# Kernel tuning notes

Hardware: AMD Instinct MI355X
Metric: run time of the kernel (lower is better)

The kernel has to match this reference:

```python
import jax, jax.numpy as jnp
import numpy as np

B, H, W, C = 32, 224, 224, 3
HID = 64


def setup_inputs() -> dict:
    key = jax.random.key(0)
    k0, k1, k2 = jax.random.split(key, 3)
    inputs = jax.random.normal(k0, (B, H, W, C), dtype=jnp.float32)
    # Localization-net dense params. Original uses zeros init (identity transform);
    # we use small random weights plus the identity affine bias so the sampling
    # grid is a nontrivial perturbation of identity.
    w1 = jax.random.normal(k1, (H * W * C, HID), dtype=jnp.float32) * 1e-3
    b1 = jnp.zeros((HID,), dtype=jnp.float32)
    w2 = jax.random.normal(k2, (HID, 6), dtype=jnp.float32) * 1e-2
    b2 = jnp.array([1.0, 0.0, 0.0, 0.0, 1.0, 0.0], dtype=jnp.float32)
    return {"inputs": inputs, "w1": w1, "b1": b1, "w2": w2, "b2": b2}


def _bilinear_sampler(img, x_s, y_s):
    # img: [B,H,W,C]; x_s, y_s: [B,H,W] normalized coords in [-1,1]
    Bn, Hn, Wn, Cn = img.shape
    x = 0.5 * (x_s + 1.0) * (Wn - 1)
    y = 0.5 * (y_s + 1.0) * (Hn - 1)
    x0 = jnp.floor(x).astype(jnp.int32)
    x1 = x0 + 1
    y0 = jnp.floor(y).astype(jnp.int32)
    y1 = y0 + 1
    x0c = jnp.clip(x0, 0, Wn - 1)
    x1c = jnp.clip(x1, 0, Wn - 1)
    y0c = jnp.clip(y0, 0, Hn - 1)
    y1c = jnp.clip(y1, 0, Hn - 1)
    b_idx = jnp.arange(Bn, dtype=jnp.int32)[:, None, None]
    Ia = img[b_idx, y0c, x0c]  # [B,H,W,C]
    Ib = img[b_idx, y1c, x0c]
    Ic = img[b_idx, y0c, x1c]
    Id = img[b_idx, y1c, x1c]
    x0f = x0c.astype(x.dtype)
    x1f = x1c.astype(x.dtype)
    y0f = y0c.astype(y.dtype)
    y1f = y1c.astype(y.dtype)
    wa = ((x1f - x) * (y1f - y))[..., None]
    wb = ((x1f - x) * (y - y0f))[..., None]
    wc = ((x - x0f) * (y1f - y))[..., None]
    wd = ((x - x0f) * (y - y0f))[..., None]
    return wa * Ia + wb * Ib + wc * Ic + wd * Id


def reference(inputs, w1, b1, w2, b2):
    Bn, Hn, Wn, Cn = inputs.shape
    # NOTE: original keras code overwrites the conv branch with flatten(inputs),
    # so the conv/maxpool layers are dead code and omitted. Dropout is identity
    # at inference (training=False).
    flat = inputs.reshape(Bn, -1)
    h = jnp.tanh(flat @ w1 + b1)
    theta = jnp.tanh(h @ w2 + b2).reshape(Bn, 2, 3)
    # affine sampling grid over normalized target coords
    xt, yt = jnp.meshgrid(
        jnp.linspace(-1.0, 1.0, Wn, dtype=inputs.dtype),
        jnp.linspace(-1.0, 1.0, Hn, dtype=inputs.dtype),
    )  # each [H,W]
    grid = jnp.stack([xt.ravel(), yt.ravel(), jnp.ones_like(xt).ravel()])  # [3,H*W]
    batch_grid = jnp.einsum("bij,jk->bik", theta, grid).reshape(Bn, 2, Hn, Wn)
    x_s = batch_grid[:, 0]
    y_s = batch_grid[:, 1]
    return _bilinear_sampler(inputs, x_s, y_s)
```

## Files before the change

### kernel.cpp

```cpp
#include <hip/hip_runtime.h>

#define BATCH 32
#define HDIM 224
#define WDIM 224
#define CDIM 3
#define KTOT (HDIM * WDIM * CDIM)
#define HID 64
#define KCHUNK 384
#define NBLK1 (KTOT / KCHUNK)
#define PIX (HDIM * WDIM)
#define BLK3 (PIX / 256)

__global__ __launch_bounds__(256) void k1_gemm(const float* __restrict__ flat,
                                               const float* __restrict__ w1,
                                               float* __restrict__ hacc) {
    const int tid  = threadIdx.x;
    const int hid  = tid & 63;
    const int bg   = tid >> 6;
    const int bbase = bg * 8;

    float acc[8];
#pragma unroll
    for (int j = 0; j < 8; ++j) acc[j] = 0.0f;

    const int k0 = blockIdx.x * KCHUNK;
    for (int kk = 0; kk < KCHUNK; kk += 4) {
        const int k = k0 + kk;
        float4 x4[8];
#pragma unroll
        for (int j = 0; j < 8; ++j)
            x4[j] = *(const float4*)(flat + (size_t)(bbase + j) * KTOT + k);
#pragma unroll
        for (int i = 0; i < 4; ++i) {
            const float w = w1[(size_t)(k + i) * HID + hid];
#pragma unroll
            for (int j = 0; j < 8; ++j) {
                const float xv = ((const float*)&x4[j])[i];
                acc[j] = fmaf(xv, w, acc[j]);
            }
        }
    }
#pragma unroll
    for (int j = 0; j < 8; ++j)
        atomicAdd(hacc + (bbase + j) * HID + hid, acc[j]);
}

__global__ __launch_bounds__(256) void k2_head(const float* __restrict__ hacc,
                                               const float* __restrict__ b1,
                                               const float* __restrict__ w2,
                                               const float* __restrict__ b2,
                                               float* __restrict__ theta) {
    __shared__ float h[BATCH * HID];
    const int tid = threadIdx.x;
    for (int idx = tid; idx < BATCH * HID; idx += 256)
        h[idx] = tanhf(hacc[idx] + b1[idx & (HID - 1)]);
    __syncthreads();
    if (tid < BATCH * 6) {
        const int b = tid / 6;
        const int j = tid - b * 6;
        float s = b2[j];
#pragma unroll
        for (int t = 0; t < HID; ++t)
            s = fmaf(h[b * HID + t], w2[t * 6 + j], s);
        theta[tid] = tanhf(s);
    }
}

__global__ __launch_bounds__(256) void k3_sample(const float* __restrict__ img,
                                                 const float* __restrict__ theta,
                                                 float* __restrict__ out) {
    const int b   = blockIdx.x / BLK3;
    const int pix = (blockIdx.x - b * BLK3) * 256 + threadIdx.x;
    const int i   = pix / WDIM;
    const int j   = pix - i * WDIM;

    const float* th = theta + b * 6;
    const float t0 = th[0], t1 = th[1], t2 = th[2];
    const float t3 = th[3], t4 = th[4], t5 = th[5];

    const float xt = (2.0f * (float)j - (float)(WDIM - 1)) / (float)(WDIM - 1);
    const float yt = (2.0f * (float)i - (float)(HDIM - 1)) / (float)(HDIM - 1);

    const float xs = t0 * xt + t1 * yt + t2;
    const float ys = t3 * xt + t4 * yt + t5;

    const float x = 0.5f * (xs + 1.0f) * (float)(WDIM - 1);
    const float y = 0.5f * (ys + 1.0f) * (float)(HDIM - 1);

    const int x0 = (int)floorf(x);
    const int y0 = (int)floorf(y);
    const int x1 = x0 + 1;
    const int y1 = y0 + 1;

    const int x0c = min(max(x0, 0), WDIM - 1);
    const int x1c = min(max(x1, 0), WDIM - 1);
    const int y0c = min(max(y0, 0), HDIM - 1);
    const int y1c = min(max(y1, 0), HDIM - 1);

    const float x0f = (float)x0c, x1f = (float)x1c;
    const float y0f = (float)y0c, y1f = (float)y1c;

    const float wa = (x1f - x) * (y1f - y);
    const float wb = (x1f - x) * (y - y0f);
    const float wc = (x - x0f) * (y1f - y);
    const float wd = (x - x0f) * (y - y0f);

    const float* base = img + (size_t)b * KTOT;
    const float* pa = base + (size_t)(y0c * WDIM + x0c) * 3;
    const float* pb = base + (size_t)(y1c * WDIM + x0c) * 3;
    const float* pc = base + (size_t)(y0c * WDIM + x1c) * 3;
    const float* pd = base + (size_t)(y1c * WDIM + x1c) * 3;

    float* po = out + (size_t)b * KTOT + (size_t)pix * 3;
#pragma unroll
    for (int c = 0; c < 3; ++c)
        po[c] = wa * pa[c] + wb * pb[c] + wc * pc[c] + wd * pd[c];
}

extern "C" void kernel_launch(void* const* d_in, const int* in_sizes, int n_in,
                              void* d_out, int out_size, void* d_ws, size_t ws_size,
                              hipStream_t stream) {
    const float* inputs = (const float*)d_in[0];
    const float* w1     = (const float*)d_in[1];
    const float* b1     = (const float*)d_in[2];
    const float* w2     = (const float*)d_in[3];
    const float* b2     = (const float*)d_in[4];
    float* out = (float*)d_out;

    float* hacc  = (float*)d_ws;
    float* theta = hacc + BATCH * HID;

    hipMemsetAsync(hacc, 0, BATCH * HID * sizeof(float), stream);
    k1_gemm<<<NBLK1, 256, 0, stream>>>(inputs, w1, hacc);
    k2_head<<<1, 256, 0, stream>>>(hacc, b1, w2, b2, theta);
    k3_sample<<<BATCH * BLK3, 256, 0, stream>>>(inputs, theta, out);
}
```

Measured before the change: 168.5 us.

## Stage activation chunk in LDS and split K across waves in localization GEMM

The first GEMM kernel now loads a 32x128 activation tile into shared memory and has each wave own a 32-wide K slice for all 32 batches. Each w1 element is therefore read once per block instead of once per batch group, and the per-wave partial sums are reduced in LDS before the atomic adds. KCHUNK drops to 128, which triples the block count. That gives more parallelism but also more global atomics, and the 32 accumulators per thread raise register pressure.

```diff
diff --git a/kernel.cpp b/kernel.cpp
--- a/kernel.cpp
+++ b/kernel.cpp
@@ -6,43 +6,70 @@
 #define CDIM 3
 #define KTOT (HDIM * WDIM * CDIM)
 #define HID 64
-#define KCHUNK 384
+#define KCHUNK 128
 #define NBLK1 (KTOT / KCHUNK)
 #define PIX (HDIM * WDIM)
 #define BLK3 (PIX / 256)
 
-__global__ __launch_bounds__(256) void k1_gemm(const float* __restrict__ flat,
-                                               const float* __restrict__ w1,
-                                               float* __restrict__ hacc) {
+__global__ __launch_bounds__(256, 5) void k1_gemm(const float* __restrict__ flat,
+                                                  const float* __restrict__ w1,
+                                                  float* __restrict__ hacc) {
+    __shared__ float smem[8192];
     const int tid  = threadIdx.x;
-    const int hid  = tid & 63;
-    const int bg   = tid >> 6;
-    const int bbase = bg * 8;
+    const int lane = tid & 63;
+    const int wave = tid >> 6;
+    const int k0   = blockIdx.x * KCHUNK;
 
-    float acc[8];
 #pragma unroll
-    for (int j = 0; j < 8; ++j) acc[j] = 0.0f;
+    for (int t = 0; t < 4; ++t) {
+        const int idx = tid + t * 256;
+        const int b   = idx >> 5;
+        const int kq  = idx & 31;
+        const float4 v = *(const float4*)(flat + (size_t)b * KTOT + k0 + kq * 4);
+        *(float4*)(smem + b * 128 + kq * 4) = v;
+    }
+    __syncthreads();
 
-    const int k0 = blockIdx.x * KCHUNK;
-    for (int kk = 0; kk < KCHUNK; kk += 4) {
-        const int k = k0 + kk;
-        float4 x4[8];
+    float acc[32];
 #pragma unroll
-        for (int j = 0; j < 8; ++j)
-            x4[j] = *(const float4*)(flat + (size_t)(bbase + j) * KTOT + k);
+    for (int j = 0; j < 32; ++j) acc[j] = 0.0f;
+
+    const int kw = wave * 32;
 #pragma unroll
-        for (int i = 0; i < 4; ++i) {
-            const float w = w1[(size_t)(k + i) * HID + hid];
+    for (int kk = 0; kk < 32; kk += 4) {
+        const int k = k0 + kw + kk;
+        float w[4];
 #pragma unroll
-            for (int j = 0; j < 8; ++j) {
-                const float xv = ((const float*)&x4[j])[i];
-                acc[j] = fmaf(xv, w, acc[j]);
-            }
+        for (int i = 0; i < 4; ++i)
+            w[i] = w1[(size_t)(k + i) * HID + lane];
+#pragma unroll
+        for (int bg = 0; bg < 4; ++bg) {
+            float4 x[8];
+#pragma unroll
+            for (int j = 0; j < 8; ++j)
+                x[j] = *(const float4*)(smem + (bg * 8 + j) * 128 + kw + kk);
+#pragma unroll
+            for (int i = 0; i < 4; ++i)
+#pragma unroll
+                for (int j = 0; j < 8; ++j)
+                    acc[bg * 8 + j] = fmaf(((const float*)&x[j])[i], w[i],
+                                           acc[bg * 8 + j]);
         }
     }
+    __syncthreads();
+
 #pragma unroll
-    for (int j = 0; j < 8; ++j)
-        atomicAdd(hacc + (bbase + j) * HID + hid, acc[j]);
+    for (int j = 0; j < 32; ++j)
+        smem[wave * 2048 + j * 64 + lane] = acc[j];
+    __syncthreads();
+
+#pragma unroll
+    for (int t = 0; t < 8; ++t) {
+        const int idx = tid + t * 256;
+        const float s = smem[idx] + smem[2048 + idx] +
+                        smem[4096 + idx] + smem[6144 + idx];
+        atomicAdd(hacc + idx, s);
+    }
 }
 
 __global__ __launch_bounds__(256) void k2_head(const float* __restrict__ hacc,
```

New measurement: 142.0 us. -15.7%, faster.
